# Kernel tuning notes

Measured on AMD Instinct MI355X. Metric: run time of the kernel, lower is better.

## Reference

```python
import jax, jax.numpy as jnp
import numpy as np

B, S, HS = 2, 2048, 1024
H, KV, DH = 16, 4, 64
G = H // KV          # GQA group size
EPS = 1e-6
SCALE = DH ** -0.5


def rms_norm(x, w, eps=EPS):
    # normalize in fp32 over last dim, then rescale (matches MTPRMSNorm)
    xf = x.astype(jnp.float32)
    var = jnp.mean(xf * xf, axis=-1, keepdims=True)
    return (w * (xf * jax.lax.rsqrt(var + eps))).astype(x.dtype)


def setup_inputs() -> dict:
    key = jax.random.key(0)
    ks = jax.random.split(key, 6)
    return {
        "hidden_states": jax.random.normal(ks[0], (B, S, HS), jnp.float32),
        "attention_mask": jnp.zeros((1, 1, S, S), jnp.float32),
        "wq": jax.random.normal(ks[1], (HS, H * DH), jnp.float32) * 0.02,
        "wk": jax.random.normal(ks[2], (HS, KV * DH), jnp.float32) * 0.02,
        "wv": jax.random.normal(ks[3], (HS, KV * DH), jnp.float32) * 0.02,
        "wo": jax.random.normal(ks[4], (H * DH, HS), jnp.float32) * 0.02,
        "q_norm_w": jnp.ones((DH,), jnp.float32),
        "k_norm_w": jnp.ones((DH,), jnp.float32),
    }


def reference(hidden_states, attention_mask, wq, wk, wv, wo, q_norm_w, k_norm_w):
    b, s, _ = hidden_states.shape
    # projections -> per-head layout; GQA handled by broadcasting (no repeat)
    q = rms_norm((hidden_states @ wq).reshape(b, s, KV, G, DH), q_norm_w)  # [b,s,kv,g,dh]
    k = rms_norm((hidden_states @ wk).reshape(b, s, KV, DH), k_norm_w)     # [b,s,kv,dh]
    v = (hidden_states @ wv).reshape(b, s, KV, DH)                          # [b,s,kv,dh]

    # scores: [b, kv, g, q, k]
    scores = jnp.einsum("bqhgd,bkhd->bhgqk", q, k) * SCALE
    scores = scores + attention_mask[:, :, None]  # mask broadcasts over (kv,g)
    probs = jax.nn.softmax(scores.astype(jnp.float32), axis=-1).astype(q.dtype)

    out = jnp.einsum("bhgqk,bkhd->bqhgd", probs, v)  # [b,s,kv,g,dh]
    out = out.reshape(b, s, H * DH)
    return out @ wo
```

## Files before the change

kernel.cpp:

```cpp
#include <hip/hip_runtime.h>
#include <hip/hip_bf16.h>


typedef __attribute__((ext_vector_type(8))) short short8_t;
typedef __attribute__((ext_vector_type(4))) float f32x4_t;

__device__ __forceinline__ unsigned short f2bf_bits(float x) {
  unsigned int u = __float_as_uint(x);
  unsigned int r = u + 0x7fff + ((u >> 16) & 1);
  return (unsigned short)(r >> 16);
}
__device__ __forceinline__ float bf2f_bits(unsigned short b) {
  return __uint_as_float(((unsigned int)b) << 16);
}
__device__ __forceinline__ unsigned int cvt_pk_bf16(float lo, float hi) {
  unsigned int r;
  asm("v_cvt_pk_bf16_f32 %0, %1, %2" : "=v"(r) : "v"(lo), "v"(hi));
  return r;
}

__device__ __forceinline__ void async16(void* lds, const void* g) {
  __builtin_amdgcn_global_load_lds(
      (const __attribute__((address_space(1))) void*)g,
      (__attribute__((address_space(3))) void*)lds, 16, 0, 0);
}

__global__ __launch_bounds__(256) void convert_f32_bf16(
    const float* __restrict__ in, unsigned short* __restrict__ out, int n) {
  int i = (blockIdx.x * 256 + threadIdx.x) * 4;
  if (i >= n) return;
  float4 v = *(const float4*)(in + i);
  ushort4 o;
  o.x = f2bf_bits(v.x); o.y = f2bf_bits(v.y);
  o.z = f2bf_bits(v.z); o.w = f2bf_bits(v.w);
  *(ushort4*)(out + i) = o;
}

__global__ __launch_bounds__(256) void pack_weights(
    const float* __restrict__ wq, const float* __restrict__ wk,
    const float* __restrict__ wv, const float* __restrict__ wo,
    unsigned short* __restrict__ Wqkvt, unsigned short* __restrict__ Wot) {
  __shared__ unsigned short T[64][72];
  int b = blockIdx.x;
  const float* W; unsigned short* Wt; int Nsrc, n_off, bx, by;
  if (b < 256)      { W = wq; Wt = Wqkvt; Nsrc = 1024; n_off = 0;    bx = b & 15;          by = b >> 4; }
  else if (b < 320) { W = wk; Wt = Wqkvt; Nsrc = 256;  n_off = 1024; bx = (b - 256) & 3;   by = (b - 256) >> 2; }
  else if (b < 384) { W = wv; Wt = Wqkvt; Nsrc = 256;  n_off = 1280; bx = (b - 320) & 3;   by = (b - 320) >> 2; }
  else              { W = wo; Wt = Wot;   Nsrc = 1024; n_off = 0;    bx = (b - 384) & 15;  by = (b - 384) >> 4; }
  const int tn = bx * 64, tk = by * 64;
  for (int e = threadIdx.x; e < 4096; e += 256) {
    int kk = e >> 6, nn = e & 63;
    T[nn][kk] = f2bf_bits(W[(size_t)(tk + kk) * Nsrc + tn + nn]);
  }
  __syncthreads();
  for (int e = threadIdx.x; e < 4096; e += 256) {
    int nn = e >> 6, kk = e & 63;
    Wt[(size_t)(n_off + tn + nn) * 1024 + tk + kk] = T[nn][kk];
  }
}

__global__ __launch_bounds__(256) void transpose_v(
    const unsigned short* __restrict__ qkv, unsigned short* __restrict__ vt) {
  __shared__ unsigned short T[64][72];
  const int tid = threadIdx.x;
  const int st = blockIdx.x * 64, bk = blockIdx.y;
  const int b = bk >> 2, kvh = bk & 3;
  const unsigned short* src = qkv + (size_t)(b * 2048 + st) * 1536 + 1280 + kvh * 64;
  for (int e = tid; e < 4096; e += 256) {
    int s = e >> 6, d = e & 63;
    T[d][s] = src[(size_t)s * 1536 + d];
  }
  __syncthreads();
  unsigned short* dst = vt + (size_t)bk * 64 * 2048 + st;
  for (int e = tid; e < 4096; e += 256) {
    int d = e >> 6, s = e & 63;
    int p = ((s >> 5) << 5) | (((s >> 2) & 3) << 3) | (((s >> 4) & 1) << 2) | (s & 3);
    dst[(size_t)d * 2048 + p] = T[d][s];
  }
}

__global__ __launch_bounds__(256) void mask_flags(
    const float* __restrict__ mask, int* __restrict__ flags, float* __restrict__ tmax) {
  const int tid = threadIdx.x, w = tid >> 6;
  const int bq = blockIdx.y * 64, bk = blockIdx.x * 64;
  bool nz = false;
  float vmax = -INFINITY;
  #pragma unroll
  for (int i = 0; i < 4; ++i) {
    int e = (i * 256 + tid) * 4;
    int r = e >> 6, c = e & 63;
    float4 v = *(const float4*)(mask + (size_t)(bq + r) * 2048 + bk + c);
    nz |= (v.x != 0.f) | (v.y != 0.f) | (v.z != 0.f) | (v.w != 0.f);
    vmax = fmaxf(vmax, fmaxf(fmaxf(v.x, v.y), fmaxf(v.z, v.w)));
  }
  #pragma unroll
  for (int m = 1; m < 64; m <<= 1) vmax = fmaxf(vmax, __shfl_xor(vmax, m, 64));
  unsigned long long anynz = __ballot((int)nz);
  __shared__ float wm[4];
  __shared__ int wf[4];
  if ((tid & 63) == 0) { wm[w] = vmax; wf[w] = (anynz != 0ull); }
  __syncthreads();
  if (tid == 0) {
    int idx = blockIdx.y * gridDim.x + blockIdx.x;
    flags[idx] = wf[0] | wf[1] | wf[2] | wf[3];
    tmax[idx] = fmaxf(fmaxf(wm[0], wm[1]), fmaxf(wm[2], wm[3]));
  }
}

template <bool OUT_BF16, bool QKNORM>
__global__ __launch_bounds__(256) void gemm_bt(
    const unsigned short* __restrict__ A, const unsigned short* __restrict__ Bt,
    void* __restrict__ Cp, int M, int N, int K, int ldc,
    const float* __restrict__ qw, const float* __restrict__ kw) {
  __shared__ unsigned short As[128 * 32];
  __shared__ unsigned short Bs[128 * 32];
  const int tid = threadIdx.x;
  const int w = tid >> 6, l = tid & 63, lr = l & 15, lg = l >> 4;
  const int nwg = gridDim.x * gridDim.y;
  int orig = blockIdx.y * gridDim.x + blockIdx.x;
  int wgid = ((nwg & 7) == 0) ? ((orig & 7) * (nwg >> 3) + (orig >> 3)) : orig;
  const int bm = (wgid / gridDim.x) * 128, bn = (wgid % gridDim.x) * 128;
  const int wrow = (w >> 1) * 64, wcol = (w & 1) * 64;

  f32x4_t acc[4][4] = {};

  for (int k0 = 0; k0 < K; k0 += 32) {
    __syncthreads();
    #pragma unroll
    for (int i = 0; i < 2; ++i) {
      int c = i * 4 + w;
      const unsigned short* ga = A + (size_t)(bm + c * 16 + (l >> 2)) * K + k0 + (l & 3) * 8;
      async16(As + c * 512, ga);
      const unsigned short* gb = Bt + (size_t)(bn + c * 16 + (l >> 2)) * K + k0 + (l & 3) * 8;
      async16(Bs + c * 512, gb);
    }
    __syncthreads();
    short8_t af[4], bfr[4];
    #pragma unroll
    for (int m = 0; m < 4; ++m)
      af[m] = *(const short8_t*)(As + (wrow + m * 16 + lr) * 32 + lg * 8);
    #pragma unroll
    for (int n = 0; n < 4; ++n)
      bfr[n] = *(const short8_t*)(Bs + (wcol + n * 16 + lr) * 32 + lg * 8);
    #pragma unroll
    for (int m = 0; m < 4; ++m)
      #pragma unroll
      for (int n = 0; n < 4; ++n)
        acc[m][n] = __builtin_amdgcn_mfma_f32_16x16x32_bf16(af[m], bfr[n], acc[m][n], 0, 0, 0);
  }

  if constexpr (QKNORM) {
    int seg = (bn + wcol) >> 6;
    if (seg < 20) {
      const float* wseg = (seg < 16) ? qw : kw;
      float wv[4];
      #pragma unroll
      for (int n = 0; n < 4; ++n) {
        wv[n] = wseg[n * 16 + lr];
        if (seg < 16) wv[n] *= 0.125f;
      }
      #pragma unroll
      for (int m = 0; m < 4; ++m)
        #pragma unroll
        for (int j = 0; j < 4; ++j) {
          float ss = acc[m][0][j] * acc[m][0][j];
          #pragma unroll
          for (int n = 1; n < 4; ++n) ss += acc[m][n][j] * acc[m][n][j];
          #pragma unroll
          for (int x = 1; x < 16; x <<= 1) ss += __shfl_xor(ss, x, 64);
          float rinv = rsqrtf(ss * (1.0f / 64.0f) + 1e-6f);
          #pragma unroll
          for (int n = 0; n < 4; ++n) acc[m][n][j] *= rinv * wv[n];
        }
    }
  }

  #pragma unroll
  for (int m = 0; m < 4; ++m)
    #pragma unroll
    for (int n = 0; n < 4; ++n)
      #pragma unroll
      for (int j = 0; j < 4; ++j) {
        int row = bm + wrow + m * 16 + lg * 4 + j;
        int col = bn + wcol + n * 16 + lr;
        float v = acc[m][n][j];
        if (OUT_BF16) ((unsigned short*)Cp)[(size_t)row * ldc + col] = f2bf_bits(v);
        else          ((float*)Cp)[(size_t)row * ldc + col] = v;
      }
}

__global__ __launch_bounds__(256, 4) void flash_attn(
    const unsigned short* __restrict__ qkv, const unsigned short* __restrict__ vtg,
    const float* __restrict__ mask, const int* __restrict__ flags,
    const float* __restrict__ tmax, const float* __restrict__ qw,
    const float* __restrict__ kw, unsigned short* __restrict__ O) {
  int orig = blockIdx.y * 32 + blockIdx.x;
  int swz = (orig & 7) * 128 + (orig >> 3);
  const int qt = swz & 31, bh = swz >> 5;
  const int b = bh >> 4, hq = bh & 15, kvh = hq >> 2;
  const int tid = threadIdx.x, w = tid >> 6, l = tid & 63, lr = l & 15, lg = l >> 4;

  __shared__ unsigned short Ks[2][64 * 64];
  __shared__ unsigned short Vs[2][64 * 64];

  const unsigned short* Qg = qkv + (size_t)(b * 2048 + qt * 64) * 1536 + hq * 64;
  const unsigned short* Kg = qkv + (size_t)(b * 2048) * 1536 + 1024 + kvh * 64;
  const unsigned short* Vg = vtg + (size_t)(b * 4 + kvh) * 64 * 2048;
  const float* Mg = mask + (size_t)(qt * 64) * 2048;
  const int* Fp = flags + qt * 32;

  auto stage = [&](int kt2, int bi) {
    #pragma unroll
    for (int it = 0; it < 2; ++it) {
      int c = it * 256 + tid;
      int r = c >> 3, cc = (c & 7) ^ (r & 7);
      async16(&Ks[bi][it * 2048 + w * 512],
              Kg + (size_t)(kt2 * 64 + r) * 1536 + cc * 8);
      async16(&Vs[bi][it * 2048 + w * 512],
              Vg + (size_t)r * 2048 + kt2 * 64 + cc * 8);
    }
  };

  stage(0, 0);

  const float L2E = 1.44269504f;
  float pmax = fabsf(qw[l] * kw[l]);
  #pragma unroll
  for (int m = 1; m < 64; m <<= 1) pmax = fmaxf(pmax, __shfl_xor(pmax, m, 64));
  float tmx = (l < 32) ? tmax[qt * 32 + l] : -INFINITY;
  #pragma unroll
  for (int m = 1; m < 64; m <<= 1) tmx = fmaxf(tmx, __shfl_xor(tmx, m, 64));
  const float nm = -(8.0f * pmax + fmaxf(tmx, 0.0f)) * L2E;

  short8_t qf[2];
  {
    const unsigned short* qrow = Qg + (size_t)(w * 16 + lr) * 1536 + lg * 8;
    qf[0] = *(const short8_t*)(qrow);
    qf[1] = *(const short8_t*)(qrow + 32);
  }

  short8_t vb1;
  #pragma unroll
  for (int e = 0; e < 8; ++e) vb1[e] = (lr == 0) ? (short)0x3f80 : (short)0;

  f32x4_t oacc[5] = {};

  for (int kt = 0; kt < 32; ++kt) {
    __syncthreads();
    if (kt < 31) stage(kt + 1, (kt + 1) & 1);
    const int cur = kt & 1;

    f32x4_t sacc[4] = {};
    __builtin_amdgcn_s_setprio(1);
    #pragma unroll
    for (int kd = 0; kd < 2; ++kd)
      #pragma unroll
      for (int n = 0; n < 4; ++n) {
        int kr = n * 16 + lr;
        short8_t kf = *(const short8_t*)(&Ks[cur][kr * 64 + ((kd * 4 + lg) ^ (kr & 7)) * 8]);
        sacc[n] = __builtin_amdgcn_mfma_f32_16x16x32_bf16(kf, qf[kd], sacc[n], 0, 0, 0);
      }
    __builtin_amdgcn_s_setprio(0);

    const bool hasmask = Fp[kt] != 0;
    float e4[4][4];
    #pragma unroll
    for (int n = 0; n < 4; ++n) {
      if (hasmask) {
        float4 mv = *(const float4*)(Mg + (size_t)(w * 16 + lr) * 2048 + kt * 64 + n * 16 + lg * 4);
        e4[n][0] = exp2f(fmaf(sacc[n][0] + mv.x, L2E, nm));
        e4[n][1] = exp2f(fmaf(sacc[n][1] + mv.y, L2E, nm));
        e4[n][2] = exp2f(fmaf(sacc[n][2] + mv.z, L2E, nm));
        e4[n][3] = exp2f(fmaf(sacc[n][3] + mv.w, L2E, nm));
      } else {
        #pragma unroll
        for (int j = 0; j < 4; ++j)
          e4[n][j] = exp2f(fmaf(sacc[n][j], L2E, nm));
      }
    }
    short8_t pa[2];
    #pragma unroll
    for (int kd = 0; kd < 2; ++kd) {
      int4 pk;
      pk.x = (int)cvt_pk_bf16(e4[2 * kd][0],     e4[2 * kd][1]);
      pk.y = (int)cvt_pk_bf16(e4[2 * kd][2],     e4[2 * kd][3]);
      pk.z = (int)cvt_pk_bf16(e4[2 * kd + 1][0], e4[2 * kd + 1][1]);
      pk.w = (int)cvt_pk_bf16(e4[2 * kd + 1][2], e4[2 * kd + 1][3]);
      pa[kd] = *(short8_t*)&pk;
    }

    __builtin_amdgcn_s_setprio(1);
    #pragma unroll
    for (int kd = 0; kd < 2; ++kd) {
      #pragma unroll
      for (int nd = 0; nd < 4; ++nd) {
        int vr = nd * 16 + lr;
        short8_t vb = *(const short8_t*)(&Vs[cur][vr * 64 + ((kd * 4 + lg) ^ (vr & 7)) * 8]);
        oacc[nd] = __builtin_amdgcn_mfma_f32_16x16x32_bf16(pa[kd], vb, oacc[nd], 0, 0, 0);
      }
      oacc[4] = __builtin_amdgcn_mfma_f32_16x16x32_bf16(pa[kd], vb1, oacc[4], 0, 0, 0);
    }
    __builtin_amdgcn_s_setprio(0);
  }

  float rln[4];
  #pragma unroll
  for (int j = 0; j < 4; ++j) rln[j] = 1.0f / __shfl(oacc[4][j], l & 48, 64);
  #pragma unroll
  for (int nd = 0; nd < 4; ++nd)
    #pragma unroll
    for (int j = 0; j < 4; ++j) {
      size_t row = (size_t)(b * 2048 + qt * 64 + w * 16 + lg * 4 + j);
      O[row * 1024 + hq * 64 + nd * 16 + lr] = f2bf_bits(oacc[nd][j] * rln[j]);
    }
}

extern "C" void kernel_launch(void* const* d_in, const int* in_sizes, int n_in,
                              void* d_out, int out_size, void* d_ws, size_t ws_size,
                              hipStream_t stream) {
  const float* hidden = (const float*)d_in[0];
  const float* mask   = (const float*)d_in[1];
  const float* wq     = (const float*)d_in[2];
  const float* wk     = (const float*)d_in[3];
  const float* wv     = (const float*)d_in[4];
  const float* wo     = (const float*)d_in[5];
  const float* qw     = (const float*)d_in[6];
  const float* kw     = (const float*)d_in[7];

  char* ws = (char*)d_ws;
  unsigned short* Xbf   = (unsigned short*)(ws);
  unsigned short* Wqkvt = (unsigned short*)(ws +  8388608);
  unsigned short* Wot   = (unsigned short*)(ws + 11534336);
  unsigned short* QKV   = (unsigned short*)(ws + 13631488);
  unsigned short* Vtg   = Wqkvt;
  int*            flags = (int*)(ws + 10485760);
  float*          tmaxb = (float*)(ws + 10489856);
  unsigned short* Obf   = Xbf;

  convert_f32_bf16<<<4096, 256, 0, stream>>>(hidden, Xbf, 4096 * 1024);
  pack_weights<<<640, 256, 0, stream>>>(wq, wk, wv, wo, Wqkvt, Wot);

  gemm_bt<true, true><<<dim3(12, 32), 256, 0, stream>>>(
      Xbf, Wqkvt, QKV, 4096, 1536, 1024, 1536, qw, kw);
  transpose_v<<<dim3(32, 8), 256, 0, stream>>>(QKV, Vtg);
  mask_flags<<<dim3(32, 32), 256, 0, stream>>>(mask, flags, tmaxb);
  flash_attn<<<dim3(32, 32), 256, 0, stream>>>(QKV, Vtg, mask, flags, tmaxb, qw, kw, Obf);
  gemm_bt<false, false><<<dim3(8, 32), 256, 0, stream>>>(
      Obf, Wot, d_out, 4096, 1024, 1024, 1024, nullptr, nullptr);
}
```

Measured before the change: 139.8 us.

## Merge prep kernels into one launch and halve GEMM M-tile to 64

Merges the hidden-state conversion, weight packing and mask-flag kernels into a single prep launch, removing two kernel launches and the gaps between them. Both GEMMs now use 64x128 tiles instead of 128x128, doubling the number of workgroups to fill more CUs, at the cost of less data reuse per tile. The mask flags are moved into the tail of the output buffer. They are read by flash_attn before the final GEMM overwrites that region.

```diff
diff --git a/kernel.cpp b/kernel.cpp
--- a/kernel.cpp
+++ b/kernel.cpp
@@ -25,37 +25,69 @@
       (__attribute__((address_space(3))) void*)lds, 16, 0, 0);
 }
 
-__global__ __launch_bounds__(256) void convert_f32_bf16(
-    const float* __restrict__ in, unsigned short* __restrict__ out, int n) {
-  int i = (blockIdx.x * 256 + threadIdx.x) * 4;
-  if (i >= n) return;
-  float4 v = *(const float4*)(in + i);
-  ushort4 o;
-  o.x = f2bf_bits(v.x); o.y = f2bf_bits(v.y);
-  o.z = f2bf_bits(v.z); o.w = f2bf_bits(v.w);
-  *(ushort4*)(out + i) = o;
-}
-
-__global__ __launch_bounds__(256) void pack_weights(
+__global__ __launch_bounds__(256) void prep(
+    const float* __restrict__ hidden, unsigned short* __restrict__ Xbf,
     const float* __restrict__ wq, const float* __restrict__ wk,
     const float* __restrict__ wv, const float* __restrict__ wo,
-    unsigned short* __restrict__ Wqkvt, unsigned short* __restrict__ Wot) {
+    unsigned short* __restrict__ Wqkvt, unsigned short* __restrict__ Wot,
+    const float* __restrict__ mask, int* __restrict__ flags, float* __restrict__ tmax) {
   __shared__ unsigned short T[64][72];
-  int b = blockIdx.x;
-  const float* W; unsigned short* Wt; int Nsrc, n_off, bx, by;
-  if (b < 256)      { W = wq; Wt = Wqkvt; Nsrc = 1024; n_off = 0;    bx = b & 15;          by = b >> 4; }
-  else if (b < 320) { W = wk; Wt = Wqkvt; Nsrc = 256;  n_off = 1024; bx = (b - 256) & 3;   by = (b - 256) >> 2; }
-  else if (b < 384) { W = wv; Wt = Wqkvt; Nsrc = 256;  n_off = 1280; bx = (b - 320) & 3;   by = (b - 320) >> 2; }
-  else              { W = wo; Wt = Wot;   Nsrc = 1024; n_off = 0;    bx = (b - 384) & 15;  by = (b - 384) >> 4; }
-  const int tn = bx * 64, tk = by * 64;
-  for (int e = threadIdx.x; e < 4096; e += 256) {
-    int kk = e >> 6, nn = e & 63;
-    T[nn][kk] = f2bf_bits(W[(size_t)(tk + kk) * Nsrc + tn + nn]);
-  }
-  __syncthreads();
-  for (int e = threadIdx.x; e < 4096; e += 256) {
-    int nn = e >> 6, kk = e & 63;
-    Wt[(size_t)(n_off + tn + nn) * 1024 + tk + kk] = T[nn][kk];
+  const int tid = threadIdx.x;
+  int blk = blockIdx.x;
+  if (blk < 4096) {
+    int i = (blk * 256 + tid) * 4;
+    float4 v = *(const float4*)(hidden + i);
+    ushort4 o;
+    o.x = f2bf_bits(v.x); o.y = f2bf_bits(v.y);
+    o.z = f2bf_bits(v.z); o.w = f2bf_bits(v.w);
+    *(ushort4*)(Xbf + i) = o;
+    return;
+  }
+  if (blk < 4736) {
+    int b = blk - 4096;
+    const float* W; unsigned short* Wt; int Nsrc, n_off, bx, by;
+    if (b < 256)      { W = wq; Wt = Wqkvt; Nsrc = 1024; n_off = 0;    bx = b & 15;         by = b >> 4; }
+    else if (b < 320) { W = wk; Wt = Wqkvt; Nsrc = 256;  n_off = 1024; bx = (b - 256) & 3;  by = (b - 256) >> 2; }
+    else if (b < 384) { W = wv; Wt = Wqkvt; Nsrc = 256;  n_off = 1280; bx = (b - 320) & 3;  by = (b - 320) >> 2; }
+    else              { W = wo; Wt = Wot;   Nsrc = 1024; n_off = 0;    bx = (b - 384) & 15; by = (b - 384) >> 4; }
+    const int tn = bx * 64, tk = by * 64;
+    for (int e = tid; e < 4096; e += 256) {
+      int kk = e >> 6, nn = e & 63;
+      T[nn][kk] = f2bf_bits(W[(size_t)(tk + kk) * Nsrc + tn + nn]);
+    }
+    __syncthreads();
+    for (int e = tid; e < 4096; e += 256) {
+      int nn = e >> 6, kk = e & 63;
+      Wt[(size_t)(n_off + tn + nn) * 1024 + tk + kk] = T[nn][kk];
+    }
+    return;
+  }
+  {
+    int mb = blk - 4736;
+    const int bx = mb & 31, by = mb >> 5;
+    const int bq = by * 64, bk = bx * 64, w = tid >> 6;
+    bool nz = false;
+    float vmax = -INFINITY;
+    #pragma unroll
+    for (int i = 0; i < 4; ++i) {
+      int e = (i * 256 + tid) * 4;
+      int r = e >> 6, c = e & 63;
+      float4 v = *(const float4*)(mask + (size_t)(bq + r) * 2048 + bk + c);
+      nz |= (v.x != 0.f) | (v.y != 0.f) | (v.z != 0.f) | (v.w != 0.f);
+      vmax = fmaxf(vmax, fmaxf(fmaxf(v.x, v.y), fmaxf(v.z, v.w)));
+    }
+    #pragma unroll
+    for (int m = 1; m < 64; m <<= 1) vmax = fmaxf(vmax, __shfl_xor(vmax, m, 64));
+    unsigned long long anynz = __ballot((int)nz);
+    __shared__ float wm[4];
+    __shared__ int wf[4];
+    if ((tid & 63) == 0) { wm[w] = vmax; wf[w] = (anynz != 0ull); }
+    __syncthreads();
+    if (tid == 0) {
+      int idx = by * 32 + bx;
+      flags[idx] = wf[0] | wf[1] | wf[2] | wf[3];
+      tmax[idx] = fmaxf(fmaxf(wm[0], wm[1]), fmaxf(wm[2], wm[3]));
+    }
   }
 }
 
@@ -79,71 +111,45 @@
   }
 }
 
-__global__ __launch_bounds__(256) void mask_flags(
-    const float* __restrict__ mask, int* __restrict__ flags, float* __restrict__ tmax) {
-  const int tid = threadIdx.x, w = tid >> 6;
-  const int bq = blockIdx.y * 64, bk = blockIdx.x * 64;
-  bool nz = false;
-  float vmax = -INFINITY;
-  #pragma unroll
-  for (int i = 0; i < 4; ++i) {
-    int e = (i * 256 + tid) * 4;
-    int r = e >> 6, c = e & 63;
-    float4 v = *(const float4*)(mask + (size_t)(bq + r) * 2048 + bk + c);
-    nz |= (v.x != 0.f) | (v.y != 0.f) | (v.z != 0.f) | (v.w != 0.f);
-    vmax = fmaxf(vmax, fmaxf(fmaxf(v.x, v.y), fmaxf(v.z, v.w)));
-  }
-  #pragma unroll
-  for (int m = 1; m < 64; m <<= 1) vmax = fmaxf(vmax, __shfl_xor(vmax, m, 64));
-  unsigned long long anynz = __ballot((int)nz);
-  __shared__ float wm[4];
-  __shared__ int wf[4];
-  if ((tid & 63) == 0) { wm[w] = vmax; wf[w] = (anynz != 0ull); }
-  __syncthreads();
-  if (tid == 0) {
-    int idx = blockIdx.y * gridDim.x + blockIdx.x;
-    flags[idx] = wf[0] | wf[1] | wf[2] | wf[3];
-    tmax[idx] = fmaxf(fmaxf(wm[0], wm[1]), fmaxf(wm[2], wm[3]));
-  }
-}
-
 template <bool OUT_BF16, bool QKNORM>
 __global__ __launch_bounds__(256) void gemm_bt(
     const unsigned short* __restrict__ A, const unsigned short* __restrict__ Bt,
     void* __restrict__ Cp, int M, int N, int K, int ldc,
     const float* __restrict__ qw, const float* __restrict__ kw) {
-  __shared__ unsigned short As[128 * 32];
+  __shared__ unsigned short As[64 * 32];
   __shared__ unsigned short Bs[128 * 32];
   const int tid = threadIdx.x;
   const int w = tid >> 6, l = tid & 63, lr = l & 15, lg = l >> 4;
   const int nwg = gridDim.x * gridDim.y;
   int orig = blockIdx.y * gridDim.x + blockIdx.x;
   int wgid = ((nwg & 7) == 0) ? ((orig & 7) * (nwg >> 3) + (orig >> 3)) : orig;
-  const int bm = (wgid / gridDim.x) * 128, bn = (wgid % gridDim.x) * 128;
-  const int wrow = (w >> 1) * 64, wcol = (w & 1) * 64;
-
-  f32x4_t acc[4][4] = {};
+  const int bm = (wgid / gridDim.x) * 64, bn = (wgid % gridDim.x) * 128;
+  const int wrow = (w >> 1) * 32, wcol = (w & 1) * 64;
+
+  f32x4_t acc[2][4] = {};
 
   for (int k0 = 0; k0 < K; k0 += 32) {
     __syncthreads();
+    {
+      const unsigned short* ga = A + (size_t)(bm + w * 16 + (l >> 2)) * K + k0 + (l & 3) * 8;
+      async16(As + w * 512, ga);
+    }
     #pragma unroll
     for (int i = 0; i < 2; ++i) {
       int c = i * 4 + w;
-      const unsigned short* ga = A + (size_t)(bm + c * 16 + (l >> 2)) * K + k0 + (l & 3) * 8;
-      async16(As + c * 512, ga);
       const unsigned short* gb = Bt + (size_t)(bn + c * 16 + (l >> 2)) * K + k0 + (l & 3) * 8;
       async16(Bs + c * 512, gb);
     }
     __syncthreads();
-    short8_t af[4], bfr[4];
-    #pragma unroll
-    for (int m = 0; m < 4; ++m)
+    short8_t af[2], bfr[4];
+    #pragma unroll
+    for (int m = 0; m < 2; ++m)
       af[m] = *(const short8_t*)(As + (wrow + m * 16 + lr) * 32 + lg * 8);
     #pragma unroll
     for (int n = 0; n < 4; ++n)
       bfr[n] = *(const short8_t*)(Bs + (wcol + n * 16 + lr) * 32 + lg * 8);
     #pragma unroll
-    for (int m = 0; m < 4; ++m)
+    for (int m = 0; m < 2; ++m)
       #pragma unroll
       for (int n = 0; n < 4; ++n)
         acc[m][n] = __builtin_amdgcn_mfma_f32_16x16x32_bf16(af[m], bfr[n], acc[m][n], 0, 0, 0);
@@ -160,7 +166,7 @@
         if (seg < 16) wv[n] *= 0.125f;
       }
       #pragma unroll
-      for (int m = 0; m < 4; ++m)
+      for (int m = 0; m < 2; ++m)
         #pragma unroll
         for (int j = 0; j < 4; ++j) {
           float ss = acc[m][0][j] * acc[m][0][j];
@@ -176,7 +182,7 @@
   }
 
   #pragma unroll
-  for (int m = 0; m < 4; ++m)
+  for (int m = 0; m < 2; ++m)
     #pragma unroll
     for (int n = 0; n < 4; ++n)
       #pragma unroll
@@ -333,18 +339,18 @@
   unsigned short* Wot   = (unsigned short*)(ws + 11534336);
   unsigned short* QKV   = (unsigned short*)(ws + 13631488);
   unsigned short* Vtg   = Wqkvt;
-  int*            flags = (int*)(ws + 10485760);
-  float*          tmaxb = (float*)(ws + 10489856);
   unsigned short* Obf   = Xbf;
 
-  convert_f32_bf16<<<4096, 256, 0, stream>>>(hidden, Xbf, 4096 * 1024);
-  pack_weights<<<640, 256, 0, stream>>>(wq, wk, wv, wo, Wqkvt, Wot);
-
-  gemm_bt<true, true><<<dim3(12, 32), 256, 0, stream>>>(
+  char* dtail = (char*)d_out + (size_t)out_size * 4 - 8192;
+  int*   flags = (int*)dtail;
+  float* tmaxb = (float*)(dtail + 4096);
+
+  prep<<<5760, 256, 0, stream>>>(hidden, Xbf, wq, wk, wv, wo, Wqkvt, Wot, mask, flags, tmaxb);
+
+  gemm_bt<true, true><<<dim3(12, 64), 256, 0, stream>>>(
       Xbf, Wqkvt, QKV, 4096, 1536, 1024, 1536, qw, kw);
   transpose_v<<<dim3(32, 8), 256, 0, stream>>>(QKV, Vtg);
-  mask_flags<<<dim3(32, 32), 256, 0, stream>>>(mask, flags, tmaxb);
   flash_attn<<<dim3(32, 32), 256, 0, stream>>>(QKV, Vtg, mask, flags, tmaxb, qw, kw, Obf);
-  gemm_bt<false, false><<<dim3(8, 32), 256, 0, stream>>>(
+  gemm_bt<false, false><<<dim3(8, 64), 256, 0, stream>>>(
       Obf, Wot, d_out, 4096, 1024, 1024, 1024, nullptr, nullptr);
 }
```

Result: faster. 127.9 us (-8.5%).
